# Kernel optimization log

Hardware: AMD Instinct MI355X
Metric: run time of the kernel (lower is better)

## Reference

```python
import jax, jax.numpy as jnp
import numpy as np

N_NODES = 100000
N_EDGES = 1600000
NFEAT, NHID, NCLASS = 128, 64, 16


def setup_inputs() -> dict:
    key = jax.random.key(0)
    ks = jax.random.split(key, 6)
    x = jax.random.normal(ks[0], (N_NODES, NFEAT), dtype=jnp.float32)
    src = jax.random.randint(ks[1], (N_EDGES,), 0, N_NODES)
    dst = jax.random.randint(ks[2], (N_EDGES,), 0, N_NODES)
    # Glorot-ish init for the two GraphConv weights, zero bias (DGL default)
    W1 = jax.random.normal(ks[3], (NFEAT, NHID), dtype=jnp.float32) * (1.0 / np.sqrt(NFEAT))
    b1 = jnp.zeros((NHID,), dtype=jnp.float32)
    W2 = jax.random.normal(ks[4], (NHID, NCLASS), dtype=jnp.float32) * (1.0 / np.sqrt(NHID))
    b2 = jnp.zeros((NCLASS,), dtype=jnp.float32)
    return {"x": x, "src": src, "dst": dst, "W1": W1, "b1": b1, "W2": W2, "b2": b2}


def _graph_conv(h, W, b, src, dst, norm_src, norm_dst, n_nodes):
    """DGL GraphConv with norm='both': D_out^{-1/2} A D_in^{-1/2} h W + b.
    Apply W before aggregation when it reduces dimensionality (DGL's in>out path);
    the math is identical either way."""
    if W.shape[0] > W.shape[1]:
        h = h @ W
    h = h * norm_src[:, None]                                   # scale source feats
    agg = jax.ops.segment_sum(h[src], dst, num_segments=n_nodes)  # sparse A @ h
    agg = agg * norm_dst[:, None]
    if W.shape[0] <= W.shape[1]:
        agg = agg @ W
    return agg + b


def reference(x, src, dst, W1, b1, W2, b2):
    n = x.shape[0]
    ones = jnp.ones(src.shape, dtype=x.dtype)
    out_deg = jax.ops.segment_sum(ones, src, num_segments=n)
    in_deg = jax.ops.segment_sum(ones, dst, num_segments=n)
    norm_src = jnp.maximum(out_deg, 1.0) ** -0.5  # degree clamp as in DGL
    norm_dst = jnp.maximum(in_deg, 1.0) ** -0.5
    h = jax.nn.relu(_graph_conv(x, W1, b1, src, dst, norm_src, norm_dst, n))
    # dropout: p=0 / eval mode -> identity
    h = _graph_conv(h, W2, b2, src, dst, norm_src, norm_dst, n)
    return jax.nn.log_softmax(h, axis=1)
```

## Files before the change

kernel.cpp:

```cpp
#include <hip/hip_runtime.h>
#include <hip/hip_bf16.h>

#define NN 100000
#define NE 1600000
#define NF 128
#define NH 64
#define NC 16
#define NB1 391
#define GBIN 256
#define CHUNK 6250
#define BBUK 196
#define NCB 196
#define NGRP 1563

typedef __attribute__((ext_vector_type(8))) short short8v;
typedef __attribute__((ext_vector_type(4))) float float4v;

__device__ __forceinline__ float us2f(unsigned short u) {
    return __uint_as_float(((unsigned int)u) << 16);
}
__device__ __forceinline__ unsigned short f2us_rn(float f) {
    unsigned int u = __float_as_uint(f);
    return (unsigned short)((u + 0x7FFFu + ((u >> 16) & 1u)) >> 16);
}
__device__ __forceinline__ float ldf(const void* p, size_t i, bool f32) {
    return f32 ? ((const float*)p)[i] : us2f(((const unsigned short*)p)[i]);
}

__global__ void k_sniff(const unsigned short* __restrict__ xu, int* __restrict__ mode) {
    __shared__ int cnt;
    if (threadIdx.x == 0) cnt = 0;
    __syncthreads();
    int c = 0;
    for (int i = threadIdx.x; i < 4096; i += 256) {
        unsigned int e = (xu[i] >> 7) & 0xFFu;
        if (e >= 160u) c++;
    }
    atomicAdd(&cnt, c);
    __syncthreads();
    if (threadIdx.x == 0) mode[0] = (cnt >= 16) ? 1 : 0;
}

__global__ void k_deg(const int4* __restrict__ src4, const int4* __restrict__ dst4,
                      int* __restrict__ deg_out, int* __restrict__ deg_in) {
    int i = blockIdx.x * blockDim.x + threadIdx.x;
    if (i < NE / 4) {
        int4 s = src4[i], d = dst4[i];
        atomicAdd(&deg_out[s.x], 1); atomicAdd(&deg_out[s.y], 1);
        atomicAdd(&deg_out[s.z], 1); atomicAdd(&deg_out[s.w], 1);
        atomicAdd(&deg_in[d.x], 1);  atomicAdd(&deg_in[d.y], 1);
        atomicAdd(&deg_in[d.z], 1);  atomicAdd(&deg_in[d.w], 1);
    }
}

__global__ void k_scatter(const int* __restrict__ src, const int* __restrict__ dst,
                          int* __restrict__ cursor, int* __restrict__ srcs_sorted) {
    int e = blockIdx.x * blockDim.x + threadIdx.x;
    if (e < NE) {
        int p = atomicAdd(&cursor[dst[e]], 1);
        srcs_sorted[p] = src[e];
    }
}

__global__ void k_scan_a(const int* __restrict__ deg_in, int* __restrict__ bsum) {
    __shared__ int s[256];
    int i = blockIdx.x * 256 + threadIdx.x;
    s[threadIdx.x] = (i < NN) ? deg_in[i] : 0;
    __syncthreads();
    for (int off = 128; off > 0; off >>= 1) {
        if (threadIdx.x < off) s[threadIdx.x] += s[threadIdx.x + off];
        __syncthreads();
    }
    if (threadIdx.x == 0) bsum[blockIdx.x] = s[0];
}

__global__ void k_scan_b(const int* __restrict__ bsum, int* __restrict__ boff) {
    __shared__ int s[512];
    int t = threadIdx.x;
    s[t] = (t < NB1) ? bsum[t] : 0;
    __syncthreads();
    for (int off = 1; off < 512; off <<= 1) {
        int v = (t >= off) ? s[t - off] : 0;
        __syncthreads();
        s[t] += v;
        __syncthreads();
    }
    if (t < NB1) boff[t] = (t == 0) ? 0 : s[t - 1];
}

__global__ void k_scan_c(const int* __restrict__ deg_in, const int* __restrict__ deg_out,
                         const int* __restrict__ boff, int* __restrict__ row_off,
                         int* __restrict__ cursor, float* __restrict__ nsrc,
                         float* __restrict__ ndst) {
    __shared__ int s[256];
    int t = threadIdx.x;
    int i = blockIdx.x * 256 + t;
    int d = (i < NN) ? deg_in[i] : 0;
    s[t] = d;
    __syncthreads();
    for (int off = 1; off < 256; off <<= 1) {
        int v = (t >= off) ? s[t - off] : 0;
        __syncthreads();
        s[t] += v;
        __syncthreads();
    }
    int excl = s[t] - d + boff[blockIdx.x];
    if (i < NN) {
        row_off[i] = excl;
        cursor[i]  = excl;
        ndst[i] = rsqrtf(fmaxf((float)d, 1.0f));
        nsrc[i] = rsqrtf(fmaxf((float)deg_out[i], 1.0f));
        if (i == NN - 1) row_off[NN] = excl + d;
    }
}

__global__ __launch_bounds__(256) void k_hist2(const int* __restrict__ src,
                                               const int* __restrict__ dst,
                                               int* __restrict__ counts_d,
                                               int* __restrict__ counts_s) {
    __shared__ int hd[BBUK], hs[BBUK];
    for (int i = threadIdx.x; i < BBUK; i += 256) { hd[i] = 0; hs[i] = 0; }
    __syncthreads();
    const int g = blockIdx.x;
    const int e0 = g * CHUNK;
    for (int i = threadIdx.x; i < CHUNK; i += 256) {
        atomicAdd(&hd[dst[e0 + i] >> 9], 1);
        atomicAdd(&hs[src[e0 + i] >> 9], 1);
    }
    __syncthreads();
    for (int i = threadIdx.x; i < BBUK; i += 256) {
        counts_d[i * GBIN + g] = hd[i];
        counts_s[i * GBIN + g] = hs[i];
    }
}

__global__ void k_cs_a(const int* __restrict__ counts, int* __restrict__ csum) {
    __shared__ int s[256];
    int i = blockIdx.x * 256 + threadIdx.x;
    s[threadIdx.x] = counts[i];
    __syncthreads();
    for (int off = 128; off > 0; off >>= 1) {
        if (threadIdx.x < off) s[threadIdx.x] += s[threadIdx.x + off];
        __syncthreads();
    }
    if (threadIdx.x == 0) csum[blockIdx.x] = s[0];
}

__global__ void k_cs_b2(const int* __restrict__ csum, int* __restrict__ coff) {
    __shared__ int s[512];
    int t = threadIdx.x;
    int half = t >> 8, j = t & 255;
    s[t] = (j < NCB) ? csum[half * NCB + j] : 0;
    __syncthreads();
    for (int off = 1; off < 256; off <<= 1) {
        int v = (j >= off) ? s[t - off] : 0;
        __syncthreads();
        s[t] += v;
        __syncthreads();
    }
    if (j < NCB) coff[half * NCB + j] = (j == 0) ? 0 : s[t - 1];
}

__global__ void k_cs_c(int* __restrict__ counts, const int* __restrict__ coff) {
    __shared__ int s[256];
    int t = threadIdx.x;
    int i = blockIdx.x * 256 + t;
    int v = counts[i];
    s[t] = v;
    __syncthreads();
    for (int off = 1; off < 256; off <<= 1) {
        int u = (t >= off) ? s[t - off] : 0;
        __syncthreads();
        s[t] += u;
        __syncthreads();
    }
    counts[i] = s[t] - v + coff[blockIdx.x];
}

__global__ __launch_bounds__(256) void k_binscatter2(const int* __restrict__ src,
                                                     const int* __restrict__ dst,
                                                     const int* __restrict__ counts_d,
                                                     const int* __restrict__ counts_s,
                                                     unsigned int* __restrict__ packed,
                                                     unsigned short* __restrict__ packed2) {
    __shared__ int curd[BBUK], curs[BBUK];
    const int g = blockIdx.x;
    for (int i = threadIdx.x; i < BBUK; i += 256) {
        curd[i] = counts_d[i * GBIN + g];
        curs[i] = counts_s[i * GBIN + g];
    }
    __syncthreads();
    const int e0 = g * CHUNK;
    for (int i = threadIdx.x; i < CHUNK; i += 256) {
        int s = src[e0 + i], d = dst[e0 + i];
        int pd = atomicAdd(&curd[d >> 9], 1);
        packed[pd] = ((unsigned)s << 9) | (unsigned)(d & 511);
        int ps = atomicAdd(&curs[s >> 9], 1);
        packed2[ps] = (unsigned short)(s & 511);
    }
}

__global__ __launch_bounds__(256) void k_bdeg_out_nsrc(const int* __restrict__ counts_s,
                                                       const unsigned short* __restrict__ packed2,
                                                       float* __restrict__ nsrc) {
    __shared__ int h[512];
    const int b = blockIdx.x;
    const int n0 = b << 9;
    const int nlim = (NN - n0 < 512) ? (NN - n0) : 512;
    for (int j = threadIdx.x; j < 512; j += 256) h[j] = 0;
    __syncthreads();
    const int beg = counts_s[b * GBIN];
    const int end = (b + 1 < BBUK) ? counts_s[(b + 1) * GBIN] : NE;
    for (int i = beg + threadIdx.x; i < end; i += 256)
        atomicAdd(&h[packed2[i] & 511u], 1);
    __syncthreads();
    for (int j = threadIdx.x; j < nlim; j += 256)
        nsrc[n0 + j] = rsqrtf(fmaxf((float)h[j], 1.0f));
}

__global__ __launch_bounds__(256) void k_bucket_all(const int* __restrict__ counts_d,
                                                    const unsigned int* __restrict__ packed,
                                                    int* __restrict__ row_off,
                                                    float* __restrict__ ndst,
                                                    int* __restrict__ srcs_sorted) {
    __shared__ int h[512];
    const int b = blockIdx.x;
    const int n0 = b << 9;
    const int nlim = (NN - n0 < 512) ? (NN - n0) : 512;
    const int t = threadIdx.x;
    for (int j = t; j < 512; j += 256) h[j] = 0;
    __syncthreads();
    const int beg = counts_d[b * GBIN];
    const int end = (b + 1 < BBUK) ? counts_d[(b + 1) * GBIN] : NE;
    for (int i = beg + t; i < end; i += 256)
        atomicAdd(&h[packed[i] & 511u], 1);
    __syncthreads();
    const int degA = h[t], degB = h[t + 256];
    int offset = 1;
    #pragma unroll
    for (int d = 256; d > 0; d >>= 1) {
        __syncthreads();
        if (t < d) {
            int ai = offset * (2 * t + 1) - 1;
            int bi = offset * (2 * t + 2) - 1;
            h[bi] += h[ai];
        }
        offset <<= 1;
    }
    __syncthreads();
    if (t == 0) h[511] = 0;
    #pragma unroll
    for (int d = 1; d < 512; d <<= 1) {
        offset >>= 1;
        __syncthreads();
        if (t < d) {
            int ai = offset * (2 * t + 1) - 1;
            int bi = offset * (2 * t + 2) - 1;
            int tmp = h[ai]; h[ai] = h[bi]; h[bi] += tmp;
        }
    }
    __syncthreads();
    const int r0 = beg + h[t];
    const int r1 = beg + h[t + 256];
    if (t < nlim) {
        row_off[n0 + t] = r0;
        ndst[n0 + t] = rsqrtf(fmaxf((float)degA, 1.0f));
    }
    if (t + 256 < nlim) {
        row_off[n0 + t + 256] = r1;
        ndst[n0 + t + 256] = rsqrtf(fmaxf((float)degB, 1.0f));
    }
    if (n0 + nlim == NN && t == 0) row_off[NN] = end;
    __syncthreads();
    h[t] = r0; h[t + 256] = r1;
    __syncthreads();
    for (int i = beg + t; i < end; i += 256) {
        unsigned v = packed[i];
        int p = atomicAdd(&h[v & 511u], 1);
        srcs_sorted[p] = (int)(v >> 9);
    }
}

__global__ void k_prepW(const void* __restrict__ W1, unsigned short* __restrict__ W1f,
                        const int* __restrict__ mode) {
    const bool f32 = (mode[0] != 0);
    for (int i = threadIdx.x; i < 1024; i += 256) {
        const int kcnt = i >> 6, lane = i & 63;
        const int kc = kcnt >> 2, nt = kcnt & 3;
        const int quad = lane >> 4, col = lane & 15;
        #pragma unroll
        for (int j = 0; j < 8; ++j) {
            const size_t idx = (size_t)(kc * 32 + quad * 8 + j) * NH + nt * 16 + col;
            W1f[(size_t)i * 8 + j] = f32 ? f2us_rn(((const float*)W1)[idx])
                                         : ((const unsigned short*)W1)[idx];
        }
    }
}

__global__ __launch_bounds__(256) void k_gemm1_mfma(
    const void* __restrict__ x, const unsigned short* __restrict__ W1f,
    const float* __restrict__ nsrc, unsigned short* __restrict__ h1,
    const int* __restrict__ mode)
{
    const bool f32 = (mode[0] != 0);
    const int tid = threadIdx.x;
    const int wave = tid >> 6, lane = tid & 63;
    const int col = lane & 15, quad = lane >> 4;

    short8v bfrag[16];
    #pragma unroll
    for (int f = 0; f < 16; ++f)
        bfrag[f] = *(const short8v*)(W1f + ((size_t)f * 64 + lane) * 8);

    const int base = blockIdx.x * 64 + wave * 16;
    int arow = base + col;
    if (arow > NN - 1) arow = NN - 1;

    short8v afrag[4];
    if (f32) {
        const float4* ap = (const float4*)((const float*)x + (size_t)arow * NF);
        #pragma unroll
        for (int kc = 0; kc < 4; ++kc) {
            float4 v0 = ap[kc * 8 + quad * 2];
            float4 v1 = ap[kc * 8 + quad * 2 + 1];
            short8v af;
            af[0] = (short)f2us_rn(v0.x); af[1] = (short)f2us_rn(v0.y);
            af[2] = (short)f2us_rn(v0.z); af[3] = (short)f2us_rn(v0.w);
            af[4] = (short)f2us_rn(v1.x); af[5] = (short)f2us_rn(v1.y);
            af[6] = (short)f2us_rn(v1.z); af[7] = (short)f2us_rn(v1.w);
            afrag[kc] = af;
        }
    } else {
        const uint4* ap = (const uint4*)((const unsigned short*)x + (size_t)arow * NF);
        #pragma unroll
        for (int kc = 0; kc < 4; ++kc) {
            uint4 v = ap[kc * 4 + quad];
            afrag[kc] = *reinterpret_cast<const short8v*>(&v);
        }
    }

    float4v acc[4];
    #pragma unroll
    for (int nt = 0; nt < 4; ++nt) acc[nt] = (float4v){0.f, 0.f, 0.f, 0.f};
    #pragma unroll
    for (int kc = 0; kc < 4; ++kc)
        #pragma unroll
        for (int nt = 0; nt < 4; ++nt)
            acc[nt] = __builtin_amdgcn_mfma_f32_16x16x32_bf16(afrag[kc], bfrag[kc * 4 + nt], acc[nt], 0, 0, 0);

    #pragma unroll
    for (int reg = 0; reg < 4; ++reg) {
        const int row = base + quad * 4 + reg;
        if (row < NN) {
            const float ns = nsrc[row];
            unsigned short* hp = h1 + (size_t)row * NH + col;
            hp[0]  = f2us_rn(acc[0][reg] * ns);
            hp[16] = f2us_rn(acc[1][reg] * ns);
            hp[32] = f2us_rn(acc[2][reg] * ns);
            hp[48] = f2us_rn(acc[3][reg] * ns);
        }
    }
}

__global__ __launch_bounds__(256) void k_agg1csr(
    const int* __restrict__ row_off, const int* __restrict__ srcs,
    const unsigned short* __restrict__ h1, const float* __restrict__ ndst,
    const float* __restrict__ nsrc, const void* __restrict__ b1,
    const void* __restrict__ W2, const int* __restrict__ mode,
    unsigned short* __restrict__ h2)
{
    const bool f32 = (mode[0] != 0);
    const int lane = threadIdx.x & 63;
    const int q  = lane >> 4;
    const int li = lane & 15;

    const float bias0 = ldf(b1, 4*li+0, f32), bias1 = ldf(b1, 4*li+1, f32);
    const float bias2 = ldf(b1, 4*li+2, f32), bias3 = ldf(b1, 4*li+3, f32);
    float w2[4][4];
    #pragma unroll
    for (int j = 0; j < 4; ++j)
        #pragma unroll
        for (int m = 0; m < 4; ++m)
            w2[j][m] = ldf(W2, (size_t)(4*li+j)*NC + (q + 4*m), f32);

    const int wid = (blockIdx.x * blockDim.x + threadIdx.x) >> 6;
    const int nw  = (gridDim.x * blockDim.x) >> 6;

    for (int row = wid; row < NN; row += nw) {
        const int beg = row_off[row], end = row_off[row + 1];
        float ax = 0.f, ay = 0.f, az = 0.f, aw = 0.f;
        float bx = 0.f, by = 0.f, bz = 0.f, bw = 0.f;
        int i = beg + q;
        int s0 = (i     < end) ? srcs[i]     : 0;
        int s1 = (i + 4 < end) ? srcs[i + 4] : 0;
        while (i + 4 < end) {
            uint2 v0 = *(const uint2*)(h1 + (size_t)s0 * NH + 4*li);
            uint2 v1 = *(const uint2*)(h1 + (size_t)s1 * NH + 4*li);
            const int inext = i + 8;
            s0 = (inext     < end) ? srcs[inext]     : 0;
            s1 = (inext + 4 < end) ? srcs[inext + 4] : 0;
            ax += us2f((unsigned short)(v0.x & 0xFFFF));
            ay += us2f((unsigned short)(v0.x >> 16));
            az += us2f((unsigned short)(v0.y & 0xFFFF));
            aw += us2f((unsigned short)(v0.y >> 16));
            bx += us2f((unsigned short)(v1.x & 0xFFFF));
            by += us2f((unsigned short)(v1.x >> 16));
            bz += us2f((unsigned short)(v1.y & 0xFFFF));
            bw += us2f((unsigned short)(v1.y >> 16));
            i = inext;
        }
        if (i < end) {
            uint2 v0 = *(const uint2*)(h1 + (size_t)s0 * NH + 4*li);
            ax += us2f((unsigned short)(v0.x & 0xFFFF));
            ay += us2f((unsigned short)(v0.x >> 16));
            az += us2f((unsigned short)(v0.y & 0xFFFF));
            aw += us2f((unsigned short)(v0.y >> 16));
        }
        ax += bx; ay += by; az += bz; aw += bw;
        ax += __shfl_xor(ax, 16); ay += __shfl_xor(ay, 16);
        az += __shfl_xor(az, 16); aw += __shfl_xor(aw, 16);
        ax += __shfl_xor(ax, 32); ay += __shfl_xor(ay, 32);
        az += __shfl_xor(az, 32); aw += __shfl_xor(aw, 32);

        const float nd = ndst[row];
        const float t0 = fmaxf(fmaf(ax, nd, bias0), 0.f);
        const float t1 = fmaxf(fmaf(ay, nd, bias1), 0.f);
        const float t2 = fmaxf(fmaf(az, nd, bias2), 0.f);
        const float t3 = fmaxf(fmaf(aw, nd, bias3), 0.f);

        float p0 = fmaf(t0,w2[0][0],fmaf(t1,w2[1][0],fmaf(t2,w2[2][0],t3*w2[3][0])));
        float p1 = fmaf(t0,w2[0][1],fmaf(t1,w2[1][1],fmaf(t2,w2[2][1],t3*w2[3][1])));
        float p2 = fmaf(t0,w2[0][2],fmaf(t1,w2[1][2],fmaf(t2,w2[2][2],t3*w2[3][2])));
        float p3 = fmaf(t0,w2[0][3],fmaf(t1,w2[1][3],fmaf(t2,w2[2][3],t3*w2[3][3])));
        #pragma unroll
        for (int off = 1; off <= 8; off <<= 1) {
            p0 += __shfl_xor(p0, off);
            p1 += __shfl_xor(p1, off);
            p2 += __shfl_xor(p2, off);
            p3 += __shfl_xor(p3, off);
        }
        if (li < 4) {
            float v = (li == 0) ? p0 : (li == 1) ? p1 : (li == 2) ? p2 : p3;
            h2[(size_t)row * NC + q + 4*li] = f2us_rn(v * nsrc[row]);
        }
    }
}

__global__ __launch_bounds__(256) void k_out(
    const int* __restrict__ row_off, const int* __restrict__ srcs,
    const unsigned short* __restrict__ h2, const float* __restrict__ ndst,
    const void* __restrict__ b2, const int* __restrict__ mode,
    void* __restrict__ out)
{
    const bool f32 = (mode[0] != 0);
    const int lane = threadIdx.x & 63;
    const int q  = lane >> 3;
    const int li = lane & 7;
    const float b2v0 = ldf(b2, 2*li,   f32);
    const float b2v1 = ldf(b2, 2*li+1, f32);

    const int wid = (blockIdx.x * blockDim.x + threadIdx.x) >> 6;
    const int nw  = (gridDim.x * blockDim.x) >> 6;

    for (int r = wid; r < NN; r += nw) {
        const int beg = row_off[r], end = row_off[r + 1];
        float a0 = 0.f, a1 = 0.f, c0 = 0.f, c1 = 0.f;
        int i = beg + q;
        int s0 = (i     < end) ? srcs[i]     : 0;
        int s1 = (i + 8 < end) ? srcs[i + 8] : 0;
        while (i + 8 < end) {
            unsigned u0 = *(const unsigned*)(h2 + (size_t)s0 * NC + 2*li);
            unsigned u1 = *(const unsigned*)(h2 + (size_t)s1 * NC + 2*li);
            const int inext = i + 16;
            s0 = (inext     < end) ? srcs[inext]     : 0;
            s1 = (inext + 8 < end) ? srcs[inext + 8] : 0;
            a0 += us2f((unsigned short)(u0 & 0xFFFF));
            a1 += us2f((unsigned short)(u0 >> 16));
            c0 += us2f((unsigned short)(u1 & 0xFFFF));
            c1 += us2f((unsigned short)(u1 >> 16));
            i = inext;
        }
        if (i < end) {
            unsigned u0 = *(const unsigned*)(h2 + (size_t)s0 * NC + 2*li);
            a0 += us2f((unsigned short)(u0 & 0xFFFF));
            a1 += us2f((unsigned short)(u0 >> 16));
        }
        a0 += c0; a1 += c1;
        #pragma unroll
        for (int off = 8; off <= 32; off <<= 1) {
            a0 += __shfl_xor(a0, off);
            a1 += __shfl_xor(a1, off);
        }
        const float nd = ndst[r];
        float v0 = fmaf(a0, nd, b2v0);
        float v1 = fmaf(a1, nd, b2v1);
        float m = fmaxf(v0, v1);
        #pragma unroll
        for (int off = 1; off <= 4; off <<= 1) m = fmaxf(m, __shfl_xor(m, off));
        float sm = __expf(v0 - m) + __expf(v1 - m);
        #pragma unroll
        for (int off = 1; off <= 4; off <<= 1) sm += __shfl_xor(sm, off);
        const float lsm = __logf(sm);
        const float r0 = v0 - m - lsm, r1 = v1 - m - lsm;
        if (q == 0) {
            if (f32) {
                float2 o; o.x = r0; o.y = r1;
                *(float2*)((float*)out + (size_t)r * NC + 2*li) = o;
            } else {
                unsigned o = ((unsigned)f2us_rn(r1) << 16) | (unsigned)f2us_rn(r0);
                *(unsigned*)((unsigned short*)out + (size_t)r * NC + 2*li) = o;
            }
        }
    }
}

extern "C" void kernel_launch(void* const* d_in, const int* in_sizes, int n_in,
                              void* d_out, int out_size, void* d_ws, size_t ws_size,
                              hipStream_t stream) {
    const void* x  = d_in[0];
    const int* src = (const int*)d_in[1];
    const int* dst = (const int*)d_in[2];
    const void* W1 = d_in[3];
    const void* b1 = d_in[4];
    const void* W2 = d_in[5];
    const void* b2 = d_in[6];

    char* ws = (char*)d_ws;
    const size_t O_MODE = 0;
    const size_t O_W1F  = 1024;
    const size_t O_CNT  = O_W1F + 16384;
    const size_t O_CS   = O_CNT  + 401408;
    const size_t O_DEG  = O_CS   + 4096;
    const size_t O_NSRC = O_DEG  + 800000;
    const size_t O_NDST = O_NSRC + 400000;
    const size_t O_ROW  = O_NDST + 400000;
    const size_t O_CUR  = O_ROW  + 400128;
    const size_t O_BS   = O_CUR  + 400128;
    const size_t O_SRCS = O_BS   + 4096;
    const size_t O_H2   = O_SRCS + 6400000;
    const size_t O_H1   = O_H2   + 3200000;
    const size_t NEED = O_H1 + 12800000;
    const bool fast_csr = ws_size >= NEED;

    int*   mode     = (int*)(ws + O_MODE);
    unsigned short* W1f = (unsigned short*)(ws + O_W1F);
    int*   counts_d = (int*)(ws + O_CNT);
    int*   counts_s = counts_d + BBUK * GBIN;
    int*   csum     = (int*)(ws + O_CS);
    int*   coff     = (int*)(ws + O_CS + 2048);
    int*   deg_out  = (int*)(ws + O_DEG);
    int*   deg_in   = deg_out + NN;
    float* nsrc     = (float*)(ws + O_NSRC);
    float* ndst     = (float*)(ws + O_NDST);
    int*   row_off  = (int*)(ws + O_ROW);
    int*   cursor   = (int*)(ws + O_CUR);
    int*   bsum     = (int*)(ws + O_BS);
    int*   boff     = (int*)(ws + O_BS + 2048);
    int*   srcs_s   = (int*)(ws + O_SRCS);
    unsigned short* h2 = (unsigned short*)(ws + O_H2);
    unsigned short* h1 = (unsigned short*)(ws + O_H1);
    unsigned int*   packed  = (unsigned int*)(ws + O_H1);
    unsigned short* packed2 = (unsigned short*)(ws + O_H1 + 6400000);

    k_sniff<<<1, 256, 0, stream>>>((const unsigned short*)x, mode);
    k_prepW<<<1, 256, 0, stream>>>(W1, W1f, mode);
    if (fast_csr) {
        k_hist2<<<GBIN, 256, 0, stream>>>(src, dst, counts_d, counts_s);
        k_cs_a<<<2 * NCB, 256, 0, stream>>>(counts_d, csum);
        k_cs_b2<<<1, 512, 0, stream>>>(csum, coff);
        k_cs_c<<<2 * NCB, 256, 0, stream>>>(counts_d, coff);
        k_binscatter2<<<GBIN, 256, 0, stream>>>(src, dst, counts_d, counts_s, packed, packed2);
        k_bdeg_out_nsrc<<<BBUK, 256, 0, stream>>>(counts_s, packed2, nsrc);
        k_bucket_all<<<BBUK, 256, 0, stream>>>(counts_d, packed, row_off, ndst, srcs_s);
    } else {
        hipMemsetAsync(deg_out, 0, 2 * (size_t)NN * sizeof(int), stream);
        k_deg<<<(NE / 4 + 255) / 256, 256, 0, stream>>>((const int4*)src, (const int4*)dst, deg_out, deg_in);
        k_scan_a<<<NB1, 256, 0, stream>>>(deg_in, bsum);
        k_scan_b<<<1, 512, 0, stream>>>(bsum, boff);
        k_scan_c<<<NB1, 256, 0, stream>>>(deg_in, deg_out, boff, row_off, cursor, nsrc, ndst);
        k_scatter<<<(NE + 255) / 256, 256, 0, stream>>>(src, dst, cursor, srcs_s);
    }
    k_gemm1_mfma<<<NGRP, 256, 0, stream>>>(x, W1f, nsrc, h1, mode);
    k_agg1csr<<<2048, 256, 0, stream>>>(row_off, srcs_s, h1, ndst, nsrc, b1, W2, mode, h2);
    k_out<<<2048, 256, 0, stream>>>(row_off, srcs_s, h2, ndst, b2, mode, d_out);
}
```

Before: 278.9 us.

## Process two rows per wave in SpMM gather kernels with deeper load batching

Both the layer-1 aggregation (fused with W2) and the output aggregation kernels now have each wavefront handle a pair of rows (r and r+NHALF) at the same time. They issue more independent index and feature gathers per iteration (four per row instead of two in layer 1) and prefetch the next row pair's offsets and norms. The aim is more memory-level parallelism to hide random-gather latency. In exchange it uses more registers, which may lower occupancy, and it hardcodes NN as twice NHALF.

```diff
diff --git a/kernel.cpp b/kernel.cpp
--- a/kernel.cpp
+++ b/kernel.cpp
@@ -12,12 +12,19 @@
 #define BBUK 196
 #define NCB 196
 #define NGRP 1563
+#define NHALF 50000
 
 typedef __attribute__((ext_vector_type(8))) short short8v;
 typedef __attribute__((ext_vector_type(4))) float float4v;
 
 __device__ __forceinline__ float us2f(unsigned short u) {
     return __uint_as_float(((unsigned int)u) << 16);
+}
+__device__ __forceinline__ float bflo(unsigned u) {
+    return __uint_as_float(u << 16);
+}
+__device__ __forceinline__ float bfhi(unsigned u) {
+    return __uint_as_float(u & 0xFFFF0000u);
 }
 __device__ __forceinline__ unsigned short f2us_rn(float f) {
     unsigned int u = __float_as_uint(f);
@@ -385,64 +392,142 @@
 
     const int wid = (blockIdx.x * blockDim.x + threadIdx.x) >> 6;
     const int nw  = (gridDim.x * blockDim.x) >> 6;
-
-    for (int row = wid; row < NN; row += nw) {
-        const int beg = row_off[row], end = row_off[row + 1];
-        float ax = 0.f, ay = 0.f, az = 0.f, aw = 0.f;
-        float bx = 0.f, by = 0.f, bz = 0.f, bw = 0.f;
-        int i = beg + q;
-        int s0 = (i     < end) ? srcs[i]     : 0;
-        int s1 = (i + 4 < end) ? srcs[i + 4] : 0;
-        while (i + 4 < end) {
-            uint2 v0 = *(const uint2*)(h1 + (size_t)s0 * NH + 4*li);
-            uint2 v1 = *(const uint2*)(h1 + (size_t)s1 * NH + 4*li);
-            const int inext = i + 8;
-            s0 = (inext     < end) ? srcs[inext]     : 0;
-            s1 = (inext + 4 < end) ? srcs[inext + 4] : 0;
-            ax += us2f((unsigned short)(v0.x & 0xFFFF));
-            ay += us2f((unsigned short)(v0.x >> 16));
-            az += us2f((unsigned short)(v0.y & 0xFFFF));
-            aw += us2f((unsigned short)(v0.y >> 16));
-            bx += us2f((unsigned short)(v1.x & 0xFFFF));
-            by += us2f((unsigned short)(v1.x >> 16));
-            bz += us2f((unsigned short)(v1.y & 0xFFFF));
-            bw += us2f((unsigned short)(v1.y >> 16));
-            i = inext;
-        }
-        if (i < end) {
-            uint2 v0 = *(const uint2*)(h1 + (size_t)s0 * NH + 4*li);
-            ax += us2f((unsigned short)(v0.x & 0xFFFF));
-            ay += us2f((unsigned short)(v0.x >> 16));
-            az += us2f((unsigned short)(v0.y & 0xFFFF));
-            aw += us2f((unsigned short)(v0.y >> 16));
-        }
-        ax += bx; ay += by; az += bz; aw += bw;
-        ax += __shfl_xor(ax, 16); ay += __shfl_xor(ay, 16);
-        az += __shfl_xor(az, 16); aw += __shfl_xor(aw, 16);
-        ax += __shfl_xor(ax, 32); ay += __shfl_xor(ay, 32);
-        az += __shfl_xor(az, 32); aw += __shfl_xor(aw, 32);
-
-        const float nd = ndst[row];
-        const float t0 = fmaxf(fmaf(ax, nd, bias0), 0.f);
-        const float t1 = fmaxf(fmaf(ay, nd, bias1), 0.f);
-        const float t2 = fmaxf(fmaf(az, nd, bias2), 0.f);
-        const float t3 = fmaxf(fmaf(aw, nd, bias3), 0.f);
-
-        float p0 = fmaf(t0,w2[0][0],fmaf(t1,w2[1][0],fmaf(t2,w2[2][0],t3*w2[3][0])));
-        float p1 = fmaf(t0,w2[0][1],fmaf(t1,w2[1][1],fmaf(t2,w2[2][1],t3*w2[3][1])));
-        float p2 = fmaf(t0,w2[0][2],fmaf(t1,w2[1][2],fmaf(t2,w2[2][2],t3*w2[3][2])));
-        float p3 = fmaf(t0,w2[0][3],fmaf(t1,w2[1][3],fmaf(t2,w2[2][3],t3*w2[3][3])));
+    const uint2* __restrict__ h1v = (const uint2*)h1;
+    const unsigned uli = (unsigned)li;
+
+    int rA = wid;
+    if (rA >= NHALF) return;
+    int begA = row_off[rA],        endA = row_off[rA + 1];
+    int begB = row_off[rA + NHALF], endB = row_off[rA + NHALF + 1];
+    float ndA = ndst[rA],         nsA = nsrc[rA];
+    float ndB = ndst[rA + NHALF], nsB = nsrc[rA + NHALF];
+
+    while (rA < NHALF) {
+        const int rB = rA + NHALF;
+        const int nrA = rA + nw;
+        int nbegA = 0, nendA = 0, nbegB = 0, nendB = 0;
+        float nndA = 0.f, nnsA = 0.f, nndB = 0.f, nnsB = 0.f;
+        if (nrA < NHALF) {
+            nbegA = row_off[nrA];          nendA = row_off[nrA + 1];
+            nbegB = row_off[nrA + NHALF];  nendB = row_off[nrA + NHALF + 1];
+            nndA  = ndst[nrA];             nnsA  = nsrc[nrA];
+            nndB  = ndst[nrA + NHALF];     nnsB  = nsrc[nrA + NHALF];
+        }
+
+        float aA0 = 0.f, aA1 = 0.f, aA2 = 0.f, aA3 = 0.f;
+        float aB0 = 0.f, aB1 = 0.f, aB2 = 0.f, aB3 = 0.f;
+        const int eA1 = endA - 1, eB1 = endB - 1;
+        int iA = begA + q, iB = begB + q;
+        bool mA = iA < endA, mB = iB < endB;
+        while (mA || mB) {
+            int sA0, sA1, sA2, sA3, sB0, sB1, sB2, sB3;
+            uint2 vA0, vA1, vA2, vA3, vB0, vB1, vB2, vB3;
+            int jA1, jA2, jA3, jB1, jB2, jB3;
+            if (mA) {
+                jA1 = iA + 4; jA2 = iA + 8; jA3 = iA + 12;
+                sA0 = srcs[(unsigned)iA];
+                sA1 = srcs[(unsigned)((jA1 < endA) ? jA1 : eA1)];
+                sA2 = srcs[(unsigned)((jA2 < endA) ? jA2 : eA1)];
+                sA3 = srcs[(unsigned)((jA3 < endA) ? jA3 : eA1)];
+            }
+            if (mB) {
+                jB1 = iB + 4; jB2 = iB + 8; jB3 = iB + 12;
+                sB0 = srcs[(unsigned)iB];
+                sB1 = srcs[(unsigned)((jB1 < endB) ? jB1 : eB1)];
+                sB2 = srcs[(unsigned)((jB2 < endB) ? jB2 : eB1)];
+                sB3 = srcs[(unsigned)((jB3 < endB) ? jB3 : eB1)];
+            }
+            if (mA) {
+                vA0 = h1v[(unsigned)sA0 * 16u + uli];
+                vA1 = h1v[(unsigned)sA1 * 16u + uli];
+                vA2 = h1v[(unsigned)sA2 * 16u + uli];
+                vA3 = h1v[(unsigned)sA3 * 16u + uli];
+            }
+            if (mB) {
+                vB0 = h1v[(unsigned)sB0 * 16u + uli];
+                vB1 = h1v[(unsigned)sB1 * 16u + uli];
+                vB2 = h1v[(unsigned)sB2 * 16u + uli];
+                vB3 = h1v[(unsigned)sB3 * 16u + uli];
+            }
+            if (mA) {
+                aA0 += bflo(vA0.x); aA1 += bfhi(vA0.x);
+                aA2 += bflo(vA0.y); aA3 += bfhi(vA0.y);
+                if (jA1 < endA) {
+                    aA0 += bflo(vA1.x); aA1 += bfhi(vA1.x);
+                    aA2 += bflo(vA1.y); aA3 += bfhi(vA1.y);
+                }
+                if (jA2 < endA) {
+                    aA0 += bflo(vA2.x); aA1 += bfhi(vA2.x);
+                    aA2 += bflo(vA2.y); aA3 += bfhi(vA2.y);
+                }
+                if (jA3 < endA) {
+                    aA0 += bflo(vA3.x); aA1 += bfhi(vA3.x);
+                    aA2 += bflo(vA3.y); aA3 += bfhi(vA3.y);
+                }
+                iA += 16; mA = iA < endA;
+            }
+            if (mB) {
+                aB0 += bflo(vB0.x); aB1 += bfhi(vB0.x);
+                aB2 += bflo(vB0.y); aB3 += bfhi(vB0.y);
+                if (jB1 < endB) {
+                    aB0 += bflo(vB1.x); aB1 += bfhi(vB1.x);
+                    aB2 += bflo(vB1.y); aB3 += bfhi(vB1.y);
+                }
+                if (jB2 < endB) {
+                    aB0 += bflo(vB2.x); aB1 += bfhi(vB2.x);
+                    aB2 += bflo(vB2.y); aB3 += bfhi(vB2.y);
+                }
+                if (jB3 < endB) {
+                    aB0 += bflo(vB3.x); aB1 += bfhi(vB3.x);
+                    aB2 += bflo(vB3.y); aB3 += bfhi(vB3.y);
+                }
+                iB += 16; mB = iB < endB;
+            }
+        }
+
+        aA0 += __shfl_xor(aA0, 16); aB0 += __shfl_xor(aB0, 16);
+        aA1 += __shfl_xor(aA1, 16); aB1 += __shfl_xor(aB1, 16);
+        aA2 += __shfl_xor(aA2, 16); aB2 += __shfl_xor(aB2, 16);
+        aA3 += __shfl_xor(aA3, 16); aB3 += __shfl_xor(aB3, 16);
+        aA0 += __shfl_xor(aA0, 32); aB0 += __shfl_xor(aB0, 32);
+        aA1 += __shfl_xor(aA1, 32); aB1 += __shfl_xor(aB1, 32);
+        aA2 += __shfl_xor(aA2, 32); aB2 += __shfl_xor(aB2, 32);
+        aA3 += __shfl_xor(aA3, 32); aB3 += __shfl_xor(aB3, 32);
+
+        const float tA0 = fmaxf(fmaf(aA0, ndA, bias0), 0.f);
+        const float tA1 = fmaxf(fmaf(aA1, ndA, bias1), 0.f);
+        const float tA2 = fmaxf(fmaf(aA2, ndA, bias2), 0.f);
+        const float tA3 = fmaxf(fmaf(aA3, ndA, bias3), 0.f);
+        const float tB0 = fmaxf(fmaf(aB0, ndB, bias0), 0.f);
+        const float tB1 = fmaxf(fmaf(aB1, ndB, bias1), 0.f);
+        const float tB2 = fmaxf(fmaf(aB2, ndB, bias2), 0.f);
+        const float tB3 = fmaxf(fmaf(aB3, ndB, bias3), 0.f);
+
+        float pA0 = fmaf(tA0,w2[0][0],fmaf(tA1,w2[1][0],fmaf(tA2,w2[2][0],tA3*w2[3][0])));
+        float pA1 = fmaf(tA0,w2[0][1],fmaf(tA1,w2[1][1],fmaf(tA2,w2[2][1],tA3*w2[3][1])));
+        float pA2 = fmaf(tA0,w2[0][2],fmaf(tA1,w2[1][2],fmaf(tA2,w2[2][2],tA3*w2[3][2])));
+        float pA3 = fmaf(tA0,w2[0][3],fmaf(tA1,w2[1][3],fmaf(tA2,w2[2][3],tA3*w2[3][3])));
+        float pB0 = fmaf(tB0,w2[0][0],fmaf(tB1,w2[1][0],fmaf(tB2,w2[2][0],tB3*w2[3][0])));
+        float pB1 = fmaf(tB0,w2[0][1],fmaf(tB1,w2[1][1],fmaf(tB2,w2[2][1],tB3*w2[3][1])));
+        float pB2 = fmaf(tB0,w2[0][2],fmaf(tB1,w2[1][2],fmaf(tB2,w2[2][2],tB3*w2[3][2])));
+        float pB3 = fmaf(tB0,w2[0][3],fmaf(tB1,w2[1][3],fmaf(tB2,w2[2][3],tB3*w2[3][3])));
         #pragma unroll
         for (int off = 1; off <= 8; off <<= 1) {
-            p0 += __shfl_xor(p0, off);
-            p1 += __shfl_xor(p1, off);
-            p2 += __shfl_xor(p2, off);
-            p3 += __shfl_xor(p3, off);
+            pA0 += __shfl_xor(pA0, off); pB0 += __shfl_xor(pB0, off);
+            pA1 += __shfl_xor(pA1, off); pB1 += __shfl_xor(pB1, off);
+            pA2 += __shfl_xor(pA2, off); pB2 += __shfl_xor(pB2, off);
+            pA3 += __shfl_xor(pA3, off); pB3 += __shfl_xor(pB3, off);
         }
         if (li < 4) {
-            float v = (li == 0) ? p0 : (li == 1) ? p1 : (li == 2) ? p2 : p3;
-            h2[(size_t)row * NC + q + 4*li] = f2us_rn(v * nsrc[row]);
-        }
+            float vA = (li == 0) ? pA0 : (li == 1) ? pA1 : (li == 2) ? pA2 : pA3;
+            float vB = (li == 0) ? pB0 : (li == 1) ? pB1 : (li == 2) ? pB2 : pB3;
+            h2[(size_t)rA * NC + q + 4*li] = f2us_rn(vA * nsA);
+            h2[(size_t)rB * NC + q + 4*li] = f2us_rn(vB * nsB);
+        }
+
+        rA = nrA;
+        begA = nbegA; endA = nendA; begB = nbegB; endB = nendB;
+        ndA = nndA; nsA = nnsA; ndB = nndB; nsB = nnsB;
     }
 }
 
@@ -461,56 +546,105 @@
 
     const int wid = (blockIdx.x * blockDim.x + threadIdx.x) >> 6;
     const int nw  = (gridDim.x * blockDim.x) >> 6;
-
-    for (int r = wid; r < NN; r += nw) {
-        const int beg = row_off[r], end = row_off[r + 1];
-        float a0 = 0.f, a1 = 0.f, c0 = 0.f, c1 = 0.f;
-        int i = beg + q;
-        int s0 = (i     < end) ? srcs[i]     : 0;
-        int s1 = (i + 8 < end) ? srcs[i + 8] : 0;
-        while (i + 8 < end) {
-            unsigned u0 = *(const unsigned*)(h2 + (size_t)s0 * NC + 2*li);
-            unsigned u1 = *(const unsigned*)(h2 + (size_t)s1 * NC + 2*li);
-            const int inext = i + 16;
-            s0 = (inext     < end) ? srcs[inext]     : 0;
-            s1 = (inext + 8 < end) ? srcs[inext + 8] : 0;
-            a0 += us2f((unsigned short)(u0 & 0xFFFF));
-            a1 += us2f((unsigned short)(u0 >> 16));
-            c0 += us2f((unsigned short)(u1 & 0xFFFF));
-            c1 += us2f((unsigned short)(u1 >> 16));
-            i = inext;
-        }
-        if (i < end) {
-            unsigned u0 = *(const unsigned*)(h2 + (size_t)s0 * NC + 2*li);
-            a0 += us2f((unsigned short)(u0 & 0xFFFF));
-            a1 += us2f((unsigned short)(u0 >> 16));
-        }
-        a0 += c0; a1 += c1;
+    const unsigned* __restrict__ h2v = (const unsigned*)h2;
+    const unsigned uli = (unsigned)li;
+
+    int rA = wid;
+    if (rA >= NHALF) return;
+    int begA = row_off[rA],         endA = row_off[rA + 1];
+    int begB = row_off[rA + NHALF], endB = row_off[rA + NHALF + 1];
+    float ndA = ndst[rA], ndB = ndst[rA + NHALF];
+
+    while (rA < NHALF) {
+        const int rB = rA + NHALF;
+        const int nrA = rA + nw;
+        int nbegA = 0, nendA = 0, nbegB = 0, nendB = 0;
+        float nndA = 0.f, nndB = 0.f;
+        if (nrA < NHALF) {
+            nbegA = row_off[nrA];         nendA = row_off[nrA + 1];
+            nbegB = row_off[nrA + NHALF]; nendB = row_off[nrA + NHALF + 1];
+            nndA = ndst[nrA];             nndB = ndst[nrA + NHALF];
+        }
+
+        float aA0 = 0.f, aA1 = 0.f, aB0 = 0.f, aB1 = 0.f;
+        const int eA1 = endA - 1, eB1 = endB - 1;
+        int iA = begA + q, iB = begB + q;
+        bool mA = iA < endA, mB = iB < endB;
+        while (mA || mB) {
+            int sA0, sA1, sB0, sB1, jA1, jB1;
+            unsigned uA0, uA1, uB0, uB1;
+            if (mA) {
+                jA1 = iA + 8;
+                sA0 = srcs[(unsigned)iA];
+                sA1 = srcs[(unsigned)((jA1 < endA) ? jA1 : eA1)];
+            }
+            if (mB) {
+                jB1 = iB + 8;
+                sB0 = srcs[(unsigned)iB];
+                sB1 = srcs[(unsigned)((jB1 < endB) ? jB1 : eB1)];
+            }
+            if (mA) {
+                uA0 = h2v[(unsigned)sA0 * 8u + uli];
+                uA1 = h2v[(unsigned)sA1 * 8u + uli];
+            }
+            if (mB) {
+                uB0 = h2v[(unsigned)sB0 * 8u + uli];
+                uB1 = h2v[(unsigned)sB1 * 8u + uli];
+            }
+            if (mA) {
+                aA0 += bflo(uA0); aA1 += bfhi(uA0);
+                if (jA1 < endA) { aA0 += bflo(uA1); aA1 += bfhi(uA1); }
+                iA += 16; mA = iA < endA;
+            }
+            if (mB) {
+                aB0 += bflo(uB0); aB1 += bfhi(uB0);
+                if (jB1 < endB) { aB0 += bflo(uB1); aB1 += bfhi(uB1); }
+                iB += 16; mB = iB < endB;
+            }
+        }
         #pragma unroll
         for (int off = 8; off <= 32; off <<= 1) {
-            a0 += __shfl_xor(a0, off);
-            a1 += __shfl_xor(a1, off);
-        }
-        const float nd = ndst[r];
-        float v0 = fmaf(a0, nd, b2v0);
-        float v1 = fmaf(a1, nd, b2v1);
-        float m = fmaxf(v0, v1);
-        #pragma unroll
-        for (int off = 1; off <= 4; off <<= 1) m = fmaxf(m, __shfl_xor(m, off));
-        float sm = __expf(v0 - m) + __expf(v1 - m);
-        #pragma unroll
-        for (int off = 1; off <= 4; off <<= 1) sm += __shfl_xor(sm, off);
-        const float lsm = __logf(sm);
-        const float r0 = v0 - m - lsm, r1 = v1 - m - lsm;
+            aA0 += __shfl_xor(aA0, off); aB0 += __shfl_xor(aB0, off);
+            aA1 += __shfl_xor(aA1, off); aB1 += __shfl_xor(aB1, off);
+        }
+        float vA0 = fmaf(aA0, ndA, b2v0);
+        float vA1 = fmaf(aA1, ndA, b2v1);
+        float vB0 = fmaf(aB0, ndB, b2v0);
+        float vB1 = fmaf(aB1, ndB, b2v1);
+        float mxA = fmaxf(vA0, vA1);
+        float mxB = fmaxf(vB0, vB1);
+        #pragma unroll
+        for (int off = 1; off <= 4; off <<= 1) {
+            mxA = fmaxf(mxA, __shfl_xor(mxA, off));
+            mxB = fmaxf(mxB, __shfl_xor(mxB, off));
+        }
+        float smA = __expf(vA0 - mxA) + __expf(vA1 - mxA);
+        float smB = __expf(vB0 - mxB) + __expf(vB1 - mxB);
+        #pragma unroll
+        for (int off = 1; off <= 4; off <<= 1) {
+            smA += __shfl_xor(smA, off);
+            smB += __shfl_xor(smB, off);
+        }
+        const float lsmA = __logf(smA), lsmB = __logf(smB);
+        const float rA0 = vA0 - mxA - lsmA, rA1 = vA1 - mxA - lsmA;
+        const float rB0 = vB0 - mxB - lsmB, rB1 = vB1 - mxB - lsmB;
         if (q == 0) {
             if (f32) {
-                float2 o; o.x = r0; o.y = r1;
-                *(float2*)((float*)out + (size_t)r * NC + 2*li) = o;
+                float2 oA; oA.x = rA0; oA.y = rA1;
+                float2 oB; oB.x = rB0; oB.y = rB1;
+                *(float2*)((float*)out + (size_t)rA * NC + 2*li) = oA;
+                *(float2*)((float*)out + (size_t)rB * NC + 2*li) = oB;
             } else {
-                unsigned o = ((unsigned)f2us_rn(r1) << 16) | (unsigned)f2us_rn(r0);
-                *(unsigned*)((unsigned short*)out + (size_t)r * NC + 2*li) = o;
-            }
-        }
+                unsigned oA = ((unsigned)f2us_rn(rA1) << 16) | (unsigned)f2us_rn(rA0);
+                unsigned oB = ((unsigned)f2us_rn(rB1) << 16) | (unsigned)f2us_rn(rB0);
+                *(unsigned*)((unsigned short*)out + (size_t)rA * NC + 2*li) = oA;
+                *(unsigned*)((unsigned short*)out + (size_t)rB * NC + 2*li) = oB;
+            }
+        }
+
+        rA = nrA;
+        begA = nbegA; endA = nendA; begB = nbegB; endB = nendB;
+        ndA = nndA; ndB = nndB;
     }
 }
 
```

After: 287.2 us. 1.03x slower.
